# Optimization experiments

Measured on AMD Instinct MI355X. Metric: run time of the kernel, lower is better.

## Reference

```python
import jax, jax.numpy as jnp
import numpy as np

M, B, U, Z, H, X = 16, 2048, 16, 64, 512, 3072


def setup_inputs() -> dict:
    key = jax.random.key(0)
    ks = jax.random.split(key, 9)
    sc = lambda d: 1.0 / np.sqrt(d)
    return {
        "s": jax.random.normal(ks[0], (M, B, U + Z), dtype=jnp.float32),
        # per-mixture z2z: Linear(Z, Z); weights stored as [in, out]
        "Wzz": jax.random.normal(ks[1], (M, Z, Z), dtype=jnp.float32) * sc(Z),
        "bzz": jax.random.normal(ks[2], (M, Z), dtype=jnp.float32) * sc(Z),
        # per-mixture z2h: Linear(Z, H)
        "Wzh": jax.random.normal(ks[3], (M, Z, H), dtype=jnp.float32) * sc(Z),
        "bzh": jax.random.normal(ks[4], (M, H), dtype=jnp.float32) * sc(Z),
        # shared h2hd: Linear(H, H)
        "Whd": jax.random.normal(ks[5], (H, H), dtype=jnp.float32) * sc(H),
        "bhd": jax.random.normal(ks[6], (H,), dtype=jnp.float32) * sc(H),
        "Whx": jax.random.normal(ks[7], (H, X), dtype=jnp.float32) * sc(H),
        "bhx": jax.random.normal(ks[8], (X,), dtype=jnp.float32) * sc(H),
    }


def reference(s, Wzz, bzz, Wzh, bzh, Whd, bhd, Whx, bhx):
    # s: [M, B, U+Z]; split off z (u is unused in non-tvae mode)
    z = s[..., U:U + Z]                                   # [M, B, Z]
    # per-mixture z2z then z2h (batched over mixture dim), fused relu
    zz = jnp.einsum("mbz,mzy->mby", z, Wzz) + bzz[:, None, :]   # [M, B, Z]
    h = jax.nn.relu(jnp.einsum("mbz,mzh->mbh", zz, Wzh) + bzh[:, None, :])  # [M, B, H]
    # shared h2hd (num_layers == 1, h_dim_dec is None)
    h = jax.nn.relu(h @ Whd + bhd)                        # [M, B, H]
    xx = jax.nn.sigmoid(h @ Whx + bhx)                    # [M, B, X]
    return xx
```

## Files before the change

### kernel.cpp

```cpp
#include <hip/hip_runtime.h>
#include <stdint.h>

typedef __attribute__((ext_vector_type(4))) float f32x4;
typedef __attribute__((ext_vector_type(8))) short short8;

#define MM 16
#define BB 2048
#define UU 16
#define ZD 64
#define HH 512
#define XD 3072
#define RTOT (MM * BB)

#define MFMA16(a, b, c) __builtin_amdgcn_mfma_f32_16x16x32_bf16(a, b, c, 0, 0, 0)

static __device__ __forceinline__ unsigned short f2bf(float f) {
  union { float f; uint32_t u; } v; v.f = f;
  uint32_t r = v.u + 0x7fffu + ((v.u >> 16) & 1u);
  return (unsigned short)(r >> 16);
}

static __device__ __forceinline__ void async16(const void* g, void* l) {
  __builtin_amdgcn_global_load_lds(
      (const __attribute__((address_space(1))) uint32_t*)g,
      (__attribute__((address_space(3))) uint32_t*)l, 16, 0, 0);
}

static __device__ __forceinline__ void tr_tile(const float* __restrict__ in,
                                               unsigned short* __restrict__ out,
                                               int R, int C, int c0, int r0, int z,
                                               float (*tile)[33]) {
  const size_t base = (size_t)z * R * C;
  const int tx = threadIdx.x & 31, ty = threadIdx.x >> 5;
#pragma unroll
  for (int k = 0; k < 32; k += 8)
    tile[ty + k][tx] = in[base + (size_t)(r0 + ty + k) * C + c0 + tx];
  __syncthreads();
#pragma unroll
  for (int k = 0; k < 32; k += 8)
    out[base + (size_t)(c0 + ty + k) * R + r0 + tx] = f2bf(tile[tx][ty + k]);
}

__global__ __launch_bounds__(256) void trconv_all(
    const float* __restrict__ Wzz, const float* __restrict__ Wzh,
    const float* __restrict__ Whd, const float* __restrict__ Whx,
    unsigned short* __restrict__ wzzT, unsigned short* __restrict__ wzhT,
    unsigned short* __restrict__ whdT, unsigned short* __restrict__ whxT) {
  __shared__ float tile[32][33];
  int b = blockIdx.x;
  if (b < 64) {
    int l = b;
    tr_tile(Wzz, wzzT, 64, 64, (l & 1) * 32, ((l >> 1) & 1) * 32, l >> 2, tile);
  } else if (b < 576) {
    int l = b - 64;
    tr_tile(Wzh, wzhT, 64, 512, (l & 15) * 32, ((l >> 4) & 1) * 32, l >> 5, tile);
  } else if (b < 832) {
    int l = b - 576;
    tr_tile(Whd, whdT, 512, 512, (l & 15) * 32, (l >> 4) * 32, 0, tile);
  } else {
    int l = b - 832;
    tr_tile(Whx, whxT, 512, 3072, (l % 96) * 32, (l / 96) * 32, 0, tile);
  }
}

__global__ __launch_bounds__(256) void stage12(
    const float* __restrict__ s, const unsigned short* __restrict__ wzzT,
    const unsigned short* __restrict__ wzhT, const float* __restrict__ bzz,
    const float* __restrict__ bzh, unsigned short* __restrict__ h1) {
  __shared__ __align__(16) unsigned short zA[64 * 64];
  __shared__ __align__(16) unsigned short wzz[64 * 64];
  __shared__ __align__(16) unsigned short wbuf[2][128 * 64];
  const int m = blockIdx.y;
  const int m0r = blockIdx.x * 64;
  const int t = threadIdx.x, lane = t & 63, w = t >> 6;
  const int l15 = lane & 15, l4 = lane >> 4;

  {
    const unsigned short* g = wzzT + (size_t)m * 64 * 64;
    async16(g + t * 8, &wzz[t * 8]);
    async16(g + (t + 256) * 8, &wzz[(t + 256) * 8]);
    const unsigned short* gh = wzhT + (size_t)m * 512 * 64;
#pragma unroll
    for (int it = 0; it < 4; ++it) {
      int id = it * 256 + t;
      async16(gh + id * 8, &wbuf[0][id * 8]);
    }
  }
  const float* sb = s + ((size_t)m * BB + m0r) * (UU + ZD) + UU;
#pragma unroll
  for (int it = 0; it < 4; ++it) {
    int idx = it * 256 + t;
    int row = idx >> 4, f4 = idx & 15;
    const float4 v = *(const float4*)(sb + (size_t)row * (UU + ZD) + f4 * 4);
    ushort4 h;
    h.x = f2bf(v.x); h.y = f2bf(v.y); h.z = f2bf(v.z); h.w = f2bf(v.w);
    *(ushort4*)&zA[row * 64 + f4 * 4] = h;
  }
  __syncthreads();

  f32x4 acc1[4] = {};
#pragma unroll
  for (int ks = 0; ks < 2; ++ks) {
    short8 af, bf[4];
    af = *(const short8*)&zA[(w * 16 + l15) * 64 + ks * 32 + l4 * 8];
#pragma unroll
    for (int n = 0; n < 4; ++n)
      bf[n] = *(const short8*)&wzz[(n * 16 + l15) * 64 + ks * 32 + l4 * 8];
#pragma unroll
    for (int n = 0; n < 4; ++n) acc1[n] = MFMA16(af, bf[n], acc1[n]);
  }
  {
    const unsigned short* gh = wzhT + (size_t)m * 512 * 64 + 128 * 64;
#pragma unroll
    for (int it = 0; it < 4; ++it) {
      int id = it * 256 + t;
      async16(gh + id * 8, &wbuf[1][id * 8]);
    }
  }
  __syncthreads();
  unsigned short* zzp = zA;
#pragma unroll
  for (int n = 0; n < 4; ++n)
#pragma unroll
    for (int r = 0; r < 4; ++r) {
      int row = w * 16 + l4 * 4 + r;
      int col = n * 16 + l15;
      zzp[row * 64 + col] = f2bf(acc1[n][r] + bzz[m * 64 + col]);
    }
  __syncthreads();

  unsigned short* h1r = h1 + ((size_t)m * BB + m0r) * HH;
  for (int c = 0; c < 4; ++c) {
    f32x4 acc[8] = {};
#pragma unroll
    for (int ks = 0; ks < 2; ++ks) {
      short8 af, bf[8];
      af = *(const short8*)&zzp[(w * 16 + l15) * 64 + ks * 32 + l4 * 8];
#pragma unroll
      for (int n = 0; n < 8; ++n)
        bf[n] = *(const short8*)&wbuf[c & 1][(n * 16 + l15) * 64 + ks * 32 + l4 * 8];
#pragma unroll
      for (int n = 0; n < 8; ++n) acc[n] = MFMA16(af, bf[n], acc[n]);
    }
#pragma unroll
    for (int n = 0; n < 8; ++n)
#pragma unroll
      for (int r = 0; r < 4; ++r) {
        int row = w * 16 + l4 * 4 + r;
        int col = c * 128 + n * 16 + l15;
        float v = acc[n][r] + bzh[m * HH + col];
        h1r[(size_t)row * HH + col] = f2bf(fmaxf(v, 0.0f));
      }
    __syncthreads();
    if (c + 2 < 4) {
      const unsigned short* gh = wzhT + (size_t)m * 512 * 64 + (size_t)(c + 2) * 128 * 64;
#pragma unroll
      for (int it = 0; it < 4; ++it) {
        int id = it * 256 + t;
        async16(gh + id * 8, &wbuf[c & 1][id * 8]);
      }
    }
  }
}

template <int EPI, int Ntot, int Ktot, int MT, int NTL>
__global__ __launch_bounds__(256) void gemm_bt(
    const unsigned short* __restrict__ A,
    const unsigned short* __restrict__ BT,
    const float* __restrict__ bias,
    void* __restrict__ outp) {
  __shared__ __align__(16) unsigned short lA[2][128 * 32];
  __shared__ __align__(16) unsigned short lB[2][128 * 32];
  const int t = threadIdx.x, lane = t & 63;
  const int wid = t >> 6, wr = wid >> 1, wc = wid & 1;
  const int l15 = lane & 15, l4 = lane >> 4;

  constexpr int nwg = MT * NTL;
  constexpr int q = nwg / 8;
  const int bid = blockIdx.x;
  const int swz = (bid & 7) * q + (bid >> 3);
  const int mt = swz / NTL, nt = swz % NTL;
  const int m0 = mt * 128, n0 = nt * 128;

  const int ra = t >> 2;
  const int sa = (t & 3) * 8;

  const unsigned short* gA = A + (size_t)m0 * Ktot;
  const unsigned short* gB = BT + (size_t)n0 * Ktot;

  float bv[4];
#pragma unroll
  for (int n = 0; n < 4; ++n) bv[n] = bias[n0 + wc * 64 + n * 16 + l15];

  f32x4 acc[4][4] = {};
  constexpr int KT = Ktot / 32;

  {
    const unsigned short* a0 = gA + (size_t)ra * Ktot + sa;
    const unsigned short* b0 = gB + (size_t)ra * Ktot + sa;
    async16(a0, &lA[0][t * 8]);
    async16(a0 + (size_t)64 * Ktot, &lA[0][(t + 256) * 8]);
    async16(b0, &lB[0][t * 8]);
    async16(b0 + (size_t)64 * Ktot, &lB[0][(t + 256) * 8]);
  }
  __syncthreads();
  for (int ks = 0; ks < KT; ++ks) {
    const int cur = ks & 1;
    if (ks + 1 < KT) {
      const int ko = (ks + 1) * 32;
      const unsigned short* a0 = gA + (size_t)ra * Ktot + ko + sa;
      const unsigned short* b0 = gB + (size_t)ra * Ktot + ko + sa;
      async16(a0, &lA[cur ^ 1][t * 8]);
      async16(a0 + (size_t)64 * Ktot, &lA[cur ^ 1][(t + 256) * 8]);
      async16(b0, &lB[cur ^ 1][t * 8]);
      async16(b0 + (size_t)64 * Ktot, &lB[cur ^ 1][(t + 256) * 8]);
    }
    short8 af[4], bf[4];
#pragma unroll
    for (int i = 0; i < 4; ++i)
      af[i] = *(const short8*)&lA[cur][(wr * 64 + i * 16 + l15) * 32 + l4 * 8];
#pragma unroll
    for (int n = 0; n < 4; ++n)
      bf[n] = *(const short8*)&lB[cur][(wc * 64 + n * 16 + l15) * 32 + l4 * 8];
#pragma unroll
    for (int i = 0; i < 4; ++i)
#pragma unroll
      for (int n = 0; n < 4; ++n) acc[i][n] = MFMA16(af[i], bf[n], acc[i][n]);
    __syncthreads();
  }

#pragma unroll
  for (int i = 0; i < 4; ++i)
#pragma unroll
    for (int n = 0; n < 4; ++n) {
      const int col = n0 + wc * 64 + n * 16 + l15;
#pragma unroll
      for (int r = 0; r < 4; ++r) {
        const int row = m0 + wr * 64 + i * 16 + l4 * 4 + r;
        float v = acc[i][n][r] + bv[n];
        if (EPI == 0) {
          ((unsigned short*)outp)[(size_t)row * Ntot + col] = f2bf(fmaxf(v, 0.0f));
        } else {
          v = 1.0f / (1.0f + __expf(-v));
          ((float*)outp)[(size_t)row * Ntot + col] = v;
        }
      }
    }
}

extern "C" void kernel_launch(void* const* d_in, const int* in_sizes, int n_in,
                              void* d_out, int out_size, void* d_ws, size_t ws_size,
                              hipStream_t stream) {
  const float* s   = (const float*)d_in[0];
  const float* Wzz = (const float*)d_in[1];
  const float* bzz = (const float*)d_in[2];
  const float* Wzh = (const float*)d_in[3];
  const float* bzh = (const float*)d_in[4];
  const float* Whd = (const float*)d_in[5];
  const float* bhd = (const float*)d_in[6];
  const float* Whx = (const float*)d_in[7];
  const float* bhx = (const float*)d_in[8];
  float* out = (float*)d_out;

  char* ws = (char*)d_ws;
  unsigned short* wzzT = (unsigned short*)ws; ws += (size_t)MM * 64 * 64 * 2;
  unsigned short* wzhT = (unsigned short*)ws; ws += (size_t)MM * 512 * 64 * 2;
  unsigned short* whdT = (unsigned short*)ws; ws += (size_t)512 * 512 * 2;
  unsigned short* whxT = (unsigned short*)ws; ws += (size_t)3072 * 512 * 2;
  unsigned short* h1   = (unsigned short*)ws; ws += (size_t)RTOT * 512 * 2;
  unsigned short* h2   = (unsigned short*)ws;

  dim3 blk(256);
  trconv_all<<<dim3(2368), blk, 0, stream>>>(Wzz, Wzh, Whd, Whx, wzzT, wzhT, whdT, whxT);
  stage12<<<dim3(32, 16), blk, 0, stream>>>(s, wzzT, wzhT, bzz, bzh, h1);
  gemm_bt<0, HH, HH, 256, 4><<<dim3(1024), blk, 0, stream>>>(h1, whdT, bhd, (void*)h2);
  gemm_bt<1, XD, HH, 256, 24><<<dim3(6144), blk, 0, stream>>>(h2, whxT, bhx, (void*)out);
}
```

Measured before the change: 569.4 us.

## Triple-buffer GEMM LDS tiles with XOR swizzle and manual waitcnt barriers

Moves the shared GEMM kernel from double to triple buffering of the A/B LDS tiles, keeping two async global-to-LDS loads in flight and using explicit s_waitcnt vmcnt/s_barrier instead of __syncthreads. It also XOR-swizzles the 16-byte chunk column within each LDS row to cut bank conflicts on the MFMA fragment reads. This aims to hide global load latency and reduce LDS conflicts, at the cost of more LDS per block (possibly lower occupancy) and fragile hand-written wait counts.

```diff
diff --git a/kernel.cpp b/kernel.cpp
--- a/kernel.cpp
+++ b/kernel.cpp
@@ -169,8 +169,8 @@
     const unsigned short* __restrict__ BT,
     const float* __restrict__ bias,
     void* __restrict__ outp) {
-  __shared__ __align__(16) unsigned short lA[2][128 * 32];
-  __shared__ __align__(16) unsigned short lB[2][128 * 32];
+  __shared__ __align__(16) unsigned short lA[3][128 * 32];
+  __shared__ __align__(16) unsigned short lB[3][128 * 32];
   const int t = threadIdx.x, lane = t & 63;
   const int wid = t >> 6, wr = wid >> 1, wc = wid & 1;
   const int l15 = lane & 15, l4 = lane >> 4;
@@ -183,51 +183,66 @@
   const int m0 = mt * 128, n0 = nt * 128;
 
   const int ra = t >> 2;
-  const int sa = (t & 3) * 8;
-
-  const unsigned short* gA = A + (size_t)m0 * Ktot;
-  const unsigned short* gB = BT + (size_t)n0 * Ktot;
+  const int sx = ((t & 3) ^ ((ra >> 1) & 3)) * 8;
+
+  const unsigned short* pa = A + (size_t)(m0 + ra) * Ktot + sx;
+  const unsigned short* pb = BT + (size_t)(n0 + ra) * Ktot + sx;
 
   float bv[4];
 #pragma unroll
   for (int n = 0; n < 4; ++n) bv[n] = bias[n0 + wc * 64 + n * 16 + l15];
+
+  int aoff[4], boff[4];
+#pragma unroll
+  for (int i = 0; i < 4; ++i) {
+    int row = wr * 64 + i * 16 + l15;
+    aoff[i] = row * 32 + (l4 ^ ((row >> 1) & 3)) * 8;
+    int col = wc * 64 + i * 16 + l15;
+    boff[i] = col * 32 + (l4 ^ ((col >> 1) & 3)) * 8;
+  }
 
   f32x4 acc[4][4] = {};
   constexpr int KT = Ktot / 32;
 
-  {
-    const unsigned short* a0 = gA + (size_t)ra * Ktot + sa;
-    const unsigned short* b0 = gB + (size_t)ra * Ktot + sa;
-    async16(a0, &lA[0][t * 8]);
-    async16(a0 + (size_t)64 * Ktot, &lA[0][(t + 256) * 8]);
-    async16(b0, &lB[0][t * 8]);
-    async16(b0 + (size_t)64 * Ktot, &lB[0][(t + 256) * 8]);
-  }
-  __syncthreads();
-  for (int ks = 0; ks < KT; ++ks) {
-    const int cur = ks & 1;
-    if (ks + 1 < KT) {
-      const int ko = (ks + 1) * 32;
-      const unsigned short* a0 = gA + (size_t)ra * Ktot + ko + sa;
-      const unsigned short* b0 = gB + (size_t)ra * Ktot + ko + sa;
-      async16(a0, &lA[cur ^ 1][t * 8]);
-      async16(a0 + (size_t)64 * Ktot, &lA[cur ^ 1][(t + 256) * 8]);
-      async16(b0, &lB[cur ^ 1][t * 8]);
-      async16(b0 + (size_t)64 * Ktot, &lB[cur ^ 1][(t + 256) * 8]);
-    }
+#define STAGE(bidx)                                     \
+  do {                                                  \
+    async16(pa, &lA[bidx][t * 8]);                      \
+    async16(pa + (size_t)64 * Ktot, &lA[bidx][(t + 256) * 8]); \
+    async16(pb, &lB[bidx][t * 8]);                      \
+    async16(pb + (size_t)64 * Ktot, &lB[bidx][(t + 256) * 8]); \
+    pa += 32; pb += 32;                                 \
+  } while (0)
+
+  STAGE(0);
+  STAGE(1);
+  asm volatile("s_waitcnt vmcnt(4)" ::: "memory");
+  asm volatile("s_barrier" ::: "memory");
+
+  int r3 = 0, s3 = 2;
+  for (int kt = 0; kt < KT; ++kt) {
+    if (kt + 2 < KT) STAGE(s3);
+    const unsigned short* la = lA[r3];
+    const unsigned short* lb = lB[r3];
     short8 af[4], bf[4];
 #pragma unroll
+    for (int i = 0; i < 4; ++i) af[i] = *(const short8*)&la[aoff[i]];
+#pragma unroll
+    for (int n = 0; n < 4; ++n) bf[n] = *(const short8*)&lb[boff[n]];
+#pragma unroll
     for (int i = 0; i < 4; ++i)
-      af[i] = *(const short8*)&lA[cur][(wr * 64 + i * 16 + l15) * 32 + l4 * 8];
-#pragma unroll
-    for (int n = 0; n < 4; ++n)
-      bf[n] = *(const short8*)&lB[cur][(wc * 64 + n * 16 + l15) * 32 + l4 * 8];
-#pragma unroll
-    for (int i = 0; i < 4; ++i)
 #pragma unroll
       for (int n = 0; n < 4; ++n) acc[i][n] = MFMA16(af[i], bf[n], acc[i][n]);
-    __syncthreads();
-  }
+    if (kt + 1 < KT) {
+      if (kt + 2 < KT)
+        asm volatile("s_waitcnt vmcnt(4) lgkmcnt(0)" ::: "memory");
+      else
+        asm volatile("s_waitcnt vmcnt(0) lgkmcnt(0)" ::: "memory");
+      asm volatile("s_barrier" ::: "memory");
+    }
+    r3 = (r3 == 2) ? 0 : r3 + 1;
+    s3 = (s3 == 2) ? 0 : s3 + 1;
+  }
+#undef STAGE
 
 #pragma unroll
   for (int i = 0; i < 4; ++i)
```

New measurement: 568.5 us. Within noise of the previous version (-0.1%).
